# Optimization experiments

Measured on AMD Instinct MI355X. Metric: run time of the kernel, lower is better.

## Reference

```python
import jax, jax.numpy as jnp
import numpy as np

# Lee-oscillator hyperparameters (from __init__)
A = (0.6, 0.6, -0.5, 0.5, -0.6, -0.6, -0.5, 0.5)
K = 50.0
N = 50  # number of iterations (torch draws randint(1, N+1); we fix N for determinism)


def setup_inputs() -> dict:
    key = jax.random.key(0)
    x = jax.random.normal(key, (4, 1024, 512), dtype=jnp.float32)
    return {"x": x}


def reference(x) -> jnp.ndarray:
    a = A
    # initial state: u0 = z0 = 0.2, v0 = 0 (broadcast to x's shape)
    u0 = jnp.full_like(x, 0.2)
    v0 = jnp.zeros_like(x)
    z0 = jnp.full_like(x, 0.2)
    # loop-invariant terms, computed once
    decay = jnp.exp(-K * x * x)  # exp(-K * x^2)
    w = jnp.tanh(x)

    def step(carry, _):
        u, v, z = carry
        u_n = jnp.tanh(a[0] * u - a[1] * v + a[2] * z + a[3] * x)
        v_n = jnp.tanh(a[6] * z - a[4] * u - a[5] * v + a[7] * x)
        z_n = (v_n - u_n) * decay + w
        return (u_n, v_n, z_n), None

    (u, v, z), _ = jax.lax.scan(step, (u0, v0, z0), None, length=N - 1)
    return z  # z[-1] of the torch recurrence
```

## Files before the change

### kernel.cpp

```cpp
#include <hip/hip_runtime.h>


#define NITER 49
#define X2_THR 0.1242922f
#define BLOCK_THREADS 1024
#define BLOCK_ELEMS 4096
#define SLOW_CAP 1536

typedef unsigned long long u64;

__device__ __forceinline__ float exp2f_hw(float a) { return __builtin_amdgcn_exp2f(a); }
__device__ __forceinline__ float rcpf_hw(float a) { return __builtin_amdgcn_rcpf(a); }

__device__ __forceinline__ float tanh_acc(float x) {
    const float T = 2.885390081777927f;
    float e = exp2f_hw(T * x);
    float d = e + 1.0f;
    float r = rcpf_hw(d);
    r = r * __builtin_fmaf(-d, r, 2.0f);
    return __builtin_fmaf(-2.0f, r, 1.0f);
}

__global__ __launch_bounds__(BLOCK_THREADS, 8) void lee_block(const float* __restrict__ x,
                                                              float* __restrict__ out,
                                                              long long n) {
    __shared__ float s_x[SLOW_CAP];
    __shared__ unsigned short s_idx[SLOW_CAP];
    __shared__ unsigned s_cnt;

    const int tid  = threadIdx.x;
    const int wid  = tid >> 6;
    const int lane = tid & 63;
    const long long bbase = (long long)blockIdx.x * BLOCK_ELEMS;
    if (tid == 0) s_cnt = 0;
    __syncthreads();

    const u64 lt = (1ull << lane) - 1ull;
    const long long e4 = bbase + (long long)tid * 4;

    float xs[4];
    bool valid[4];
    if (e4 + 3 < n) {
        float4 xv = *reinterpret_cast<const float4*>(x + e4);
        xs[0] = xv.x; xs[1] = xv.y; xs[2] = xv.z; xs[3] = xv.w;
        valid[0] = valid[1] = valid[2] = valid[3] = true;
    } else {
#pragma unroll
        for (int j = 0; j < 4; ++j) {
            valid[j] = (e4 + j) < n;
            xs[j] = valid[j] ? x[e4 + j] : 10.0f;
        }
    }

    float ts[4];
#pragma unroll
    for (int j = 0; j < 4; ++j) ts[j] = tanh_acc(xs[j]);
    if (e4 + 3 < n) {
        float4 ov; ov.x = ts[0]; ov.y = ts[1]; ov.z = ts[2]; ov.w = ts[3];
        *reinterpret_cast<float4*>(out + e4) = ov;
    } else {
#pragma unroll
        for (int j = 0; j < 4; ++j) if (valid[j]) out[e4 + j] = ts[j];
    }

#pragma unroll
    for (int j = 0; j < 4; ++j) {
        float xx = xs[j];
        bool slow = valid[j] && (xx * xx <= X2_THR);
        u64 m = __ballot(slow);
        unsigned wtot = (unsigned)__popcll(m);
        unsigned wbase = 0;
        if (lane == 0 && wtot) wbase = atomicAdd(&s_cnt, wtot);
        wbase = __shfl(wbase, 0, 64);
        if (slow) {
            unsigned pos = wbase + (unsigned)__popcll(m & lt);
            if (pos < SLOW_CAP) {
                s_x[pos] = xx;
                s_idx[pos] = (unsigned short)(tid * 4 + j);
            }
        }
    }
    __syncthreads();

    unsigned cnt = s_cnt;
    if (cnt > SLOW_CAP) cnt = SLOW_CAP;
    unsigned nch = (cnt + 127) >> 7;

    const float T   = 2.885390081777927f;
    const float C05 = 0.5f * T;
    const float C06 = 0.6f * T;
    const float NK  = -72.13475204444817f;

    for (unsigned ch = wid; ch < nch; ch += BLOCK_THREADS / 64) {
        unsigned r0 = ch * 128 + lane, r1 = r0 + 64;
        bool v0 = r0 < cnt, v1 = r1 < cnt;
        float X[2];
        X[0] = v0 ? s_x[r0] : 10.0f;
        X[1] = v1 ? s_x[r1] : 10.0f;

        float pxT[2], d2[2], wv[2], U[2], V[2], Z[2];
#pragma unroll
        for (int k = 0; k < 2; ++k) {
            pxT[k] = C05 * X[k];
            d2[k]  = 2.0f * exp2f_hw(NK * X[k] * X[k]);
            wv[k]  = tanh_acc(X[k]);
            U[k] = 0.2f; V[k] = 0.0f; Z[k] = 0.2f;
        }
#pragma unroll 7
        for (int it = 0; it < NITER; ++it) {
#pragma unroll
            for (int k = 0; k < 2; ++k) {
                float cT  = __builtin_fmaf(-C05, Z[k], pxT[k]);
                float sT  = __builtin_fmaf(C06, U[k], cT);
                float auT = __builtin_fmaf(-C06, V[k], sT);
                float avT = __builtin_fmaf(C06, V[k], sT);
                float EU  = exp2f_hw(auT);
                float EV  = exp2f_hw(avT);
                float A   = EU + 1.0f;
                float B   = EV + 1.0f;
                float RP  = rcpf_hw(A * B);
                float R2  = -2.0f * RP;
                U[k] = __builtin_fmaf(B, R2, 1.0f);
                V[k] = __builtin_fmaf(A, R2, 1.0f);
                Z[k] = __builtin_fmaf((B - A) * RP, d2[k], wv[k]);
            }
        }
        if (v0) out[bbase + s_idx[r0]] = Z[0];
        if (v1) out[bbase + s_idx[r1]] = Z[1];
    }
}

extern "C" void kernel_launch(void* const* d_in, const int* in_sizes, int n_in,
                              void* d_out, int out_size, void* d_ws, size_t ws_size,
                              hipStream_t stream) {
    const float* x = (const float*)d_in[0];
    float* out = (float*)d_out;
    long long n = in_sizes[0];
    long long blocks = (n + BLOCK_ELEMS - 1) / BLOCK_ELEMS;
    lee_block<<<(int)blocks, BLOCK_THREADS, 0, stream>>>(x, out, n);
}
```

Baseline: 77.63 us.

## Split into classify and global compacted-iteration kernels for load balance

Replaces the single per-block kernel with three launches. A zero kernel resets a counter, a classify kernel writes the cheap tanh outputs and appends slow-element global indices into a workspace list through one global atomic per block, and a persistent iterate kernel runs the 49-step recurrence on the compacted list with 4 elements per thread. The aim is to balance the expensive recurrence evenly across the whole GPU instead of leaving it tied to each block's local slow count, and to raise ILP. In exchange it adds two extra launches, global index traffic and gathered loads of x. A per-element fallback kernel is kept for when the workspace is too small.

```diff
diff --git a/kernel.cpp b/kernel.cpp
--- a/kernel.cpp
+++ b/kernel.cpp
@@ -21,15 +21,20 @@
     return __builtin_fmaf(-2.0f, r, 1.0f);
 }
 
-__global__ __launch_bounds__(BLOCK_THREADS, 8) void lee_block(const float* __restrict__ x,
-                                                              float* __restrict__ out,
-                                                              long long n) {
-    __shared__ float s_x[SLOW_CAP];
+__global__ void lee_zero(unsigned* __restrict__ ctr) {
+    if (threadIdx.x == 0) ctr[0] = 0;
+}
+
+__global__ __launch_bounds__(BLOCK_THREADS, 8) void lee_classify(const float* __restrict__ x,
+                                                                 float* __restrict__ out,
+                                                                 unsigned* __restrict__ ctr,
+                                                                 unsigned* __restrict__ gidx,
+                                                                 long long n) {
     __shared__ unsigned short s_idx[SLOW_CAP];
     __shared__ unsigned s_cnt;
+    __shared__ unsigned s_base;
 
     const int tid  = threadIdx.x;
-    const int wid  = tid >> 6;
     const int lane = tid & 63;
     const long long bbase = (long long)blockIdx.x * BLOCK_ELEMS;
     if (tid == 0) s_cnt = 0;
@@ -74,33 +79,49 @@
         wbase = __shfl(wbase, 0, 64);
         if (slow) {
             unsigned pos = wbase + (unsigned)__popcll(m & lt);
-            if (pos < SLOW_CAP) {
-                s_x[pos] = xx;
-                s_idx[pos] = (unsigned short)(tid * 4 + j);
-            }
+            if (pos < SLOW_CAP) s_idx[pos] = (unsigned short)(tid * 4 + j);
         }
     }
     __syncthreads();
 
     unsigned cnt = s_cnt;
     if (cnt > SLOW_CAP) cnt = SLOW_CAP;
-    unsigned nch = (cnt + 127) >> 7;
+    if (tid == 0) s_base = atomicAdd(ctr, cnt);
+    __syncthreads();
+    unsigned gb = s_base;
+
+    for (unsigned t = tid; t < cnt; t += BLOCK_THREADS)
+        gidx[gb + t] = (unsigned)(bbase + (long long)s_idx[t]);
+}
+
+__global__ __launch_bounds__(256, 8) void lee_iter(const float* __restrict__ x,
+                                                   float* __restrict__ out,
+                                                   const unsigned* __restrict__ ctr,
+                                                   const unsigned* __restrict__ gidx) {
+    const unsigned total = ctr[0];
+    const unsigned stride = gridDim.x * 256u * 4u;
 
     const float T   = 2.885390081777927f;
     const float C05 = 0.5f * T;
     const float C06 = 0.6f * T;
     const float NK  = -72.13475204444817f;
 
-    for (unsigned ch = wid; ch < nch; ch += BLOCK_THREADS / 64) {
-        unsigned r0 = ch * 128 + lane, r1 = r0 + 64;
-        bool v0 = r0 < cnt, v1 = r1 < cnt;
-        float X[2];
-        X[0] = v0 ? s_x[r0] : 10.0f;
-        X[1] = v1 ? s_x[r1] : 10.0f;
-
-        float pxT[2], d2[2], wv[2], U[2], V[2], Z[2];
-#pragma unroll
-        for (int k = 0; k < 2; ++k) {
+    for (unsigned g0 = (blockIdx.x * 256u + threadIdx.x) * 4u; g0 < total; g0 += stride) {
+        unsigned id[4];
+        bool vld[4];
+        float X[4];
+#pragma unroll
+        for (int k = 0; k < 4; ++k) {
+            unsigned g = g0 + k;
+            vld[k] = g < total;
+            id[k] = vld[k] ? gidx[g] : 0u;
+        }
+#pragma unroll
+        for (int k = 0; k < 4; ++k) X[k] = vld[k] ? x[id[k]] : 10.0f;
+
+        float pxT[4], d2[4], wv[4], U[4], V[4], Z[4];
+#pragma unroll
+        for (int k = 0; k < 4; ++k) {
             pxT[k] = C05 * X[k];
             d2[k]  = 2.0f * exp2f_hw(NK * X[k] * X[k]);
             wv[k]  = tanh_acc(X[k]);
@@ -109,7 +130,7 @@
 #pragma unroll 7
         for (int it = 0; it < NITER; ++it) {
 #pragma unroll
-            for (int k = 0; k < 2; ++k) {
+            for (int k = 0; k < 4; ++k) {
                 float cT  = __builtin_fmaf(-C05, Z[k], pxT[k]);
                 float sT  = __builtin_fmaf(C06, U[k], cT);
                 float auT = __builtin_fmaf(-C06, V[k], sT);
@@ -125,9 +146,41 @@
                 Z[k] = __builtin_fmaf((B - A) * RP, d2[k], wv[k]);
             }
         }
-        if (v0) out[bbase + s_idx[r0]] = Z[0];
-        if (v1) out[bbase + s_idx[r1]] = Z[1];
-    }
+#pragma unroll
+        for (int k = 0; k < 4; ++k) if (vld[k]) out[id[k]] = Z[k];
+    }
+}
+
+__global__ __launch_bounds__(256) void lee_mono(const float* __restrict__ x,
+                                                float* __restrict__ out, long long n) {
+    long long i = (long long)blockIdx.x * blockDim.x + threadIdx.x;
+    if (i >= n) return;
+    float xx = x[i];
+    if (xx * xx > X2_THR) { out[i] = tanh_acc(xx); return; }
+    const float T   = 2.885390081777927f;
+    const float C05 = 0.5f * T;
+    const float C06 = 0.6f * T;
+    const float NK  = -72.13475204444817f;
+    float pxT = C05 * xx;
+    float d2  = 2.0f * exp2f_hw(NK * xx * xx);
+    float w   = tanh_acc(xx);
+    float u = 0.2f, v = 0.0f, z = 0.2f;
+    for (int it = 0; it < NITER; ++it) {
+        float cT  = __builtin_fmaf(-C05, z, pxT);
+        float sT  = __builtin_fmaf(C06, u, cT);
+        float auT = __builtin_fmaf(-C06, v, sT);
+        float avT = __builtin_fmaf(C06, v, sT);
+        float EU  = exp2f_hw(auT);
+        float EV  = exp2f_hw(avT);
+        float A   = EU + 1.0f;
+        float B   = EV + 1.0f;
+        float RP  = rcpf_hw(A * B);
+        float R2  = -2.0f * RP;
+        u = __builtin_fmaf(B, R2, 1.0f);
+        v = __builtin_fmaf(A, R2, 1.0f);
+        z = __builtin_fmaf((B - A) * RP, d2, w);
+    }
+    out[i] = z;
 }
 
 extern "C" void kernel_launch(void* const* d_in, const int* in_sizes, int n_in,
@@ -136,6 +189,15 @@
     const float* x = (const float*)d_in[0];
     float* out = (float*)d_out;
     long long n = in_sizes[0];
-    long long blocks = (n + BLOCK_ELEMS - 1) / BLOCK_ELEMS;
-    lee_block<<<(int)blocks, BLOCK_THREADS, 0, stream>>>(x, out, n);
-}
+    size_t need = 64 + (size_t)n * sizeof(unsigned);
+    if (ws_size >= need) {
+        unsigned* ctr  = (unsigned*)d_ws;
+        unsigned* gidx = (unsigned*)((char*)d_ws + 64);
+        long long blocks = (n + BLOCK_ELEMS - 1) / BLOCK_ELEMS;
+        lee_zero<<<1, 64, 0, stream>>>(ctr);
+        lee_classify<<<(int)blocks, BLOCK_THREADS, 0, stream>>>(x, out, ctr, gidx, n);
+        lee_iter<<<576, 256, 0, stream>>>(x, out, ctr, gidx);
+    } else {
+        lee_mono<<<(int)((n + 255) / 256), 256, 0, stream>>>(x, out, n);
+    }
+}
```

New measurement: 90.01 us. +16.0%, slower.
